# Kernel tuning notes

Measured on AMD Instinct MI355X. Metric: run time of the kernel, lower is better.

The kernel has to match this reference:

```python
import jax, jax.numpy as jnp
import numpy as np

IN_CH, OUT_CH, KS = 64, 128, 3
GRID, DEG = 8, 3
STRIDE, PAD = 1, 1
SIZE = IN_CH * KS * KS            # 576
NCOEF = GRID + DEG                # 11
GRID_RANGE = (-1.0, 1.0)


def _xavier_uniform(key, shape):
    fan_out, fan_in = shape
    a = float(np.sqrt(6.0 / (fan_in + fan_out)))
    return jax.random.uniform(key, shape, minval=-a, maxval=a, dtype=jnp.float32)


def setup_inputs() -> dict:
    key = jax.random.key(0)
    k1, k2, k3 = jax.random.split(key, 3)
    x = jax.random.normal(k1, (8, IN_CH, 32, 32), dtype=jnp.float32)
    # non-trainable knot grid, one row per unfolded feature
    knots = jnp.tile(jnp.linspace(GRID_RANGE[0], GRID_RANGE[1], GRID + 1, dtype=jnp.float32)[None, :], (SIZE, 1))
    coeff = 0.1 * jax.random.normal(k2, (OUT_CH, SIZE, NCOEF), dtype=jnp.float32)
    base_weights = _xavier_uniform(k3, (OUT_CH, SIZE))
    spline_weights = jnp.ones((OUT_CH, SIZE), dtype=jnp.float32)
    return {"x": x, "knots": knots, "coeff": coeff,
            "base_weights": base_weights, "spline_weights": spline_weights}


def bspline_basis(x, grid, k):
    # x: (S, P) evaluation points; grid: (S, G+1) knots. Returns (S, G+k, P).
    h = (grid[:, -1:] - grid[:, :1]) / (grid.shape[1] - 1)
    left = grid[:, :1] - h * jnp.arange(k, 0, -1, dtype=x.dtype)
    right = grid[:, -1:] + h * jnp.arange(1, k + 1, dtype=x.dtype)
    g = jnp.concatenate([left, grid, right], axis=1)  # (S, G+1+2k)
    xe = x[:, None, :]
    B = ((xe >= g[:, :-1, None]) & (xe < g[:, 1:, None])).astype(x.dtype)
    for d in range(1, k + 1):  # de Boor recursion over fixed degree
        B = ((xe - g[:, :-(d + 1), None]) / (g[:, d:-1, None] - g[:, :-(d + 1), None]) * B[:, :-1]
             + (g[:, d + 1:, None] - xe) / (g[:, d + 1:, None] - g[:, 1:-d, None]) * B[:, 1:])
    return B


def _unfold(x):
    # torch F.unfold with channel-major (c, kh, kw) feature ordering
    N, C, H, W = x.shape
    xp = jnp.pad(x, ((0, 0), (0, 0), (PAD, PAD), (PAD, PAD)))
    Hp = (H + 2 * PAD - KS) // STRIDE + 1
    Wp = (W + 2 * PAD - KS) // STRIDE + 1
    patches = jnp.stack([xp[:, :, i:i + STRIDE * Hp:STRIDE, j:j + STRIDE * Wp:STRIDE]
                         for i in range(KS) for j in range(KS)], axis=2)  # (N, C, KS*KS, Hp, Wp)
    L = Hp * Wp
    u = patches.reshape(N, SIZE, L)              # (N, size, L)
    u = jnp.transpose(u, (1, 0, 2)).reshape(SIZE, N * L)  # (size, N*L), col = n*L + l
    return u, Hp, Wp


def reference(x, knots, coeff, base_weights, spline_weights):
    N = x.shape[0]
    u, Hp, Wp = _unfold(x)                                   # (size, P)
    base = base_weights @ jax.nn.silu(u)                     # (Cout, P)
    B = bspline_basis(u, knots, DEG)                         # (size, ncoef, P)
    eff = spline_weights[:, :, None] * coeff                 # (Cout, size, ncoef)
    spl = jnp.einsum('csj,sjp->cp', eff, B)                  # (Cout, P)
    out = (base + spl).reshape(OUT_CH, N, Hp, Wp)
    return jnp.transpose(out, (1, 0, 2, 3))                  # (N, Cout, Hp, Wp)
```

## Files before the change

kernel.cpp:

```cpp
#include <hip/hip_runtime.h>


typedef __attribute__((ext_vector_type(8))) short bf16x8;
typedef __attribute__((ext_vector_type(4))) float f32x4;
typedef __attribute__((ext_vector_type(16))) float f32x16;
typedef __attribute__((ext_vector_type(4))) unsigned short u16x4;

#define WSWZ_BYTES 1769472
#define PHI_OFF    WSWZ_BYTES
#define PHI_BYTES  14205696

__device__ __forceinline__ short f2bf(float f) {
    union { float f; unsigned u; } c; c.f = f;
    unsigned r = c.u + 0x7fffu + ((c.u >> 16) & 1u);
    return (short)(r >> 16);
}
__device__ __forceinline__ float bf2f(unsigned short u) {
    union { unsigned u; float f; } c; c.u = ((unsigned)u) << 16;
    return c.f;
}

__global__ void kan_prep(const float* __restrict__ coeff,
                         const float* __restrict__ basew,
                         const float* __restrict__ splw,
                         const float* __restrict__ x,
                         short* __restrict__ Wswz,
                         short* __restrict__ Phi) {
    __shared__ float coeffL[6336];
    __shared__ float basewL[576];
    __shared__ float splwL[576];
    __shared__ unsigned short xs[64 * 32];
    const int t = threadIdx.x;

    if (blockIdx.x < 272) {
        const int rowid = blockIdx.x;
        const int n     = rowid / 34;
        const int ypad  = rowid - n * 34;
        const int y     = ypad - 1;
        const bool yvalid = (y >= 0 && y < 32);

        if (yvalid) {
#pragma unroll
            for (int it = 0; it < 2; ++it) {
                int cg = t + it * 256;
                int ci = cg >> 3, q = cg & 7;
                f32x4 v = *(const f32x4*)(x + (((n * 64 + ci) * 32 + y) * 32 + q * 4));
                u16x4 p;
                p.x = (unsigned short)f2bf(v.x); p.y = (unsigned short)f2bf(v.y);
                p.z = (unsigned short)f2bf(v.z); p.w = (unsigned short)f2bf(v.w);
                *(u16x4*)&xs[ci * 32 + q * 4] = p;
            }
        }
        __syncthreads();

        const size_t rowbase = (size_t)rowid * 12 * 2176;
        for (int it = t; it < 272; it += 256) {
            int xp = it >> 3, cch = it & 7, c0 = cch << 3;
            bool interior = yvalid && (xp >= 1 && xp <= 32);
            int px = xp - 1;
            int pxc = px < 0 ? 0 : (px > 31 ? 31 : px);
            bf16x8 packs[12];
#pragma unroll
            for (int j = 0; j < 8; ++j) {
                float v = interior ? bf2f(xs[(c0 + j) * 32 + pxc]) : 0.f;
                float tt = 4.f * v + 7.f;
                int   i0 = -100;
                float b0 = 0.f, b1 = 0.f, b2 = 0.f, b3 = 0.f;
                if (tt >= 0.f && tt < 14.f) {
                    i0 = (int)tt;
                    float fr  = tt - (float)i0;
                    float omf = 1.f - fr;
                    float fr2 = fr * fr, fr3 = fr2 * fr;
                    b0 = omf * omf * omf * (1.f / 6.f);
                    b1 = (3.f * fr3 - 6.f * fr2 + 4.f) * (1.f / 6.f);
                    b2 = (-3.f * fr3 + 3.f * fr2 + 3.f * fr + 1.f) * (1.f / 6.f);
                    b3 = fr3 * (1.f / 6.f);
                }
                float silu = v * __builtin_amdgcn_rcpf(1.f + __expf(-v));
                packs[0][j] = f2bf(silu);
#pragma unroll
                for (int f = 1; f < 12; ++f) {
                    int jj = f - 1;
                    float val = 0.f;
                    val = (jj == i0 - 3) ? b0 : val;
                    val = (jj == i0 - 2) ? b1 : val;
                    val = (jj == i0 - 1) ? b2 : val;
                    val = (jj == i0    ) ? b3 : val;
                    packs[f][j] = f2bf(val);
                }
            }
            int swz = (cch ^ (xp & 7)) << 3;
#pragma unroll
            for (int f = 0; f < 12; ++f)
                *(bf16x8*)&Phi[rowbase + (size_t)f * 2176 + xp * 64 + swz] = packs[f];
        }
    } else {
        const int co = blockIdx.x - 272;
        const float* crow = coeff + co * 6336;
        for (int i = t; i < 6336; i += 256) coeffL[i] = crow[i];
        for (int i = t; i < 576; i += 256) {
            basewL[i] = basew[co * 576 + i];
            splwL[i]  = splw[co * 576 + i];
        }
        __syncthreads();
        const int cb = co >> 5, lm = co & 31;
        for (int c = t; c < 864; c += 256) {
            int kk16 = c >> 1, kh = c & 1;
            int f  = kk16 / 36;
            int rm = kk16 - f * 36;
            int tap = rm >> 2, q = rm & 3;
            bf16x8 pack;
#pragma unroll
            for (int j = 0; j < 8; ++j) {
                int ci = q * 16 + kh * 8 + j;
                int s  = ci * 9 + tap;
                float v = (f == 0) ? basewL[s] : splwL[s] * coeffL[s * 11 + (f - 1)];
                pack[j] = f2bf(v);
            }
            *(bf16x8*)(Wswz + (size_t)((kk16 * 4 + cb) * 64 + kh * 32 + lm) * 8) = pack;
        }
    }
}

__global__ __launch_bounds__(512, 1)
void kan_gemm2(const short* __restrict__ Phi,
               const short* __restrict__ Wswz,
               float* __restrict__ out) {
    __shared__ __align__(16) char Bbuf[2 * 69632];

    const int t  = threadIdx.x;
    const int w8 = t >> 6;
    const int cb = w8 & 1;
    const int fq = w8 >> 1;
    const int l  = t & 63;
    const int ln = l & 31;
    const int kh = l >> 5;

    const int ch    = blockIdx.x >> 7;
    const int ptile = blockIdx.x & 127;
    const int n     = ptile >> 4;
    const int y0    = (ptile & 15) << 1;
    const int cbg   = ch * 2 + cb;

    const char* phiB = (const char*)Phi;
    const int rowPlane = (n * 34 + y0) * 12;
    auto stage = [&](int r, int buf) {
#pragma unroll
        for (int k = 0; k < 9; ++k) {
            int i = t + k * 512;
            if (i < 4352) {
                int sfq = i / 1088;
                int rem = i - sfq * 1088;
                int row = rem / 272;
                int m   = rem - row * 272;
                const char* s = phiB + (size_t)(rowPlane + row * 12 + sfq * 3 + r) * 4352 + m * 16;
                __builtin_amdgcn_global_load_lds(
                    (const __attribute__((address_space(1))) unsigned int*)s,
                    (__attribute__((address_space(3))) unsigned int*)(Bbuf + buf * 69632 + i * 16),
                    16, 0, 0);
            }
        }
    };

    stage(0, 0);
    __syncthreads();

    f32x16 acc[2];
#pragma unroll
    for (int pb = 0; pb < 2; ++pb)
#pragma unroll
        for (int r = 0; r < 16; ++r)
            acc[pb][r] = 0.f;

    const short* Abase = Wswz + (size_t)cbg * 512 + (size_t)l * 8;

#pragma unroll 1
    for (int r = 0; r < 3; ++r) {
        const int buf = r & 1;
        if (r < 2) stage(r + 1, buf ^ 1);

        const short* B0 = (const short*)(Bbuf + buf * 69632 + fq * 17408);
        const int kbase = (fq * 3 + r) * 36;
#pragma unroll
        for (int q = 0; q < 4; ++q) {
#pragma unroll
            for (int dx = 0; dx < 3; ++dx) {
                bf16x8 a0 = *(const bf16x8*)(Abase + (size_t)(kbase + (0 * 3 + dx) * 4 + q) * 2048);
                bf16x8 a1 = *(const bf16x8*)(Abase + (size_t)(kbase + (1 * 3 + dx) * 4 + q) * 2048);
                bf16x8 a2 = *(const bf16x8*)(Abase + (size_t)(kbase + (2 * 3 + dx) * 4 + q) * 2048);
                const int c   = q * 2 + kh;
                const int key = (ln + dx) & 7;
                const int colb = (ln + dx) * 64 + ((c ^ key) << 3);
                bf16x8 b0 = *(const bf16x8*)&B0[0 * 2176 + colb];
                bf16x8 b1 = *(const bf16x8*)&B0[1 * 2176 + colb];
                bf16x8 b2 = *(const bf16x8*)&B0[2 * 2176 + colb];
                bf16x8 b3 = *(const bf16x8*)&B0[3 * 2176 + colb];
                acc[0] = __builtin_amdgcn_mfma_f32_32x32x16_bf16(a0, b0, acc[0], 0, 0, 0);
                acc[1] = __builtin_amdgcn_mfma_f32_32x32x16_bf16(a0, b1, acc[1], 0, 0, 0);
                acc[0] = __builtin_amdgcn_mfma_f32_32x32x16_bf16(a1, b1, acc[0], 0, 0, 0);
                acc[1] = __builtin_amdgcn_mfma_f32_32x32x16_bf16(a1, b2, acc[1], 0, 0, 0);
                acc[0] = __builtin_amdgcn_mfma_f32_32x32x16_bf16(a2, b2, acc[0], 0, 0, 0);
                acc[1] = __builtin_amdgcn_mfma_f32_32x32x16_bf16(a2, b3, acc[1], 0, 0, 0);
            }
        }
        __syncthreads();
    }

    float* ex = (float*)Bbuf;
    if (fq != 0) {
        const int slot = (fq - 1) * 2 + cb;
#pragma unroll
        for (int pb = 0; pb < 2; ++pb)
#pragma unroll
            for (int r = 0; r < 16; ++r) {
                int v = pb * 16 + r;
                ex[slot * 2048 + l * 32 + ((v + l) & 31)] = acc[pb][r];
            }
    }
    __syncthreads();
    if (fq == 0) {
#pragma unroll
        for (int s = 0; s < 3; ++s)
#pragma unroll
            for (int pb = 0; pb < 2; ++pb)
#pragma unroll
                for (int r = 0; r < 16; ++r) {
                    int v = pb * 16 + r;
                    acc[pb][r] += ex[(s * 2 + cb) * 2048 + l * 32 + ((v + l) & 31)];
                }

#pragma unroll
        for (int pb = 0; pb < 2; ++pb) {
            int y = y0 + pb;
#pragma unroll
            for (int r = 0; r < 16; ++r) {
                int row = (r & 3) + 8 * (r >> 2) + 4 * kh;
                int co  = cbg * 32 + row;
                out[((size_t)(n * 128 + co) * 32 + y) * 32 + ln] = acc[pb][r];
            }
        }
    }
}

extern "C" void kernel_launch(void* const* d_in, const int* in_sizes, int n_in,
                              void* d_out, int out_size, void* d_ws, size_t ws_size,
                              hipStream_t stream) {
    const float* x     = (const float*)d_in[0];
    const float* coeff = (const float*)d_in[2];
    const float* basew = (const float*)d_in[3];
    const float* splw  = (const float*)d_in[4];
    float* out = (float*)d_out;

    short* Wswz = (short*)d_ws;
    short* Phi  = (short*)((char*)d_ws + PHI_OFF);

    kan_prep<<<400, 256, 0, stream>>>(coeff, basew, splw, x, Wswz, Phi);
    kan_gemm2<<<256, 512, 0, stream>>>(Phi, Wswz, out);
}
```

Before: 102.7 us.

## Fuse basis expansion into GEMM kernel, dropping the materialized Phi buffer

Each GEMM block now loads its four padded input rows, converts them to bf16 in shared memory, and computes the SiLU and B-spline basis values on the fly into LDS for each of the three feature rounds. The prep kernel that wrote a ~14 MB Phi tensor to global memory and the async global-to-LDS staging are removed, leaving a weights-only prep kernel. This cuts global memory traffic but moves basis computation into the GEMM blocks and serializes it with the MFMA loop, since there is no double buffering, and each block recomputes halo rows.

```diff
diff --git a/kernel.cpp b/kernel.cpp
--- a/kernel.cpp
+++ b/kernel.cpp
@@ -6,10 +6,6 @@
 typedef __attribute__((ext_vector_type(16))) float f32x16;
 typedef __attribute__((ext_vector_type(4))) unsigned short u16x4;
 
-#define WSWZ_BYTES 1769472
-#define PHI_OFF    WSWZ_BYTES
-#define PHI_BYTES  14205696
-
 __device__ __forceinline__ short f2bf(float f) {
     union { float f; unsigned u; } c; c.f = f;
     unsigned r = c.u + 0x7fffu + ((c.u >> 16) & 1u);
@@ -20,49 +16,96 @@
     return c.f;
 }
 
-__global__ void kan_prep(const float* __restrict__ coeff,
-                         const float* __restrict__ basew,
-                         const float* __restrict__ splw,
-                         const float* __restrict__ x,
-                         short* __restrict__ Wswz,
-                         short* __restrict__ Phi) {
+__global__ void kan_weights(const float* __restrict__ coeff,
+                            const float* __restrict__ basew,
+                            const float* __restrict__ splw,
+                            short* __restrict__ Wswz) {
     __shared__ float coeffL[6336];
     __shared__ float basewL[576];
     __shared__ float splwL[576];
-    __shared__ unsigned short xs[64 * 32];
-    const int t = threadIdx.x;
-
-    if (blockIdx.x < 272) {
-        const int rowid = blockIdx.x;
-        const int n     = rowid / 34;
-        const int ypad  = rowid - n * 34;
-        const int y     = ypad - 1;
-        const bool yvalid = (y >= 0 && y < 32);
-
-        if (yvalid) {
-#pragma unroll
-            for (int it = 0; it < 2; ++it) {
-                int cg = t + it * 256;
-                int ci = cg >> 3, q = cg & 7;
-                f32x4 v = *(const f32x4*)(x + (((n * 64 + ci) * 32 + y) * 32 + q * 4));
-                u16x4 p;
-                p.x = (unsigned short)f2bf(v.x); p.y = (unsigned short)f2bf(v.y);
-                p.z = (unsigned short)f2bf(v.z); p.w = (unsigned short)f2bf(v.w);
-                *(u16x4*)&xs[ci * 32 + q * 4] = p;
-            }
-        }
-        __syncthreads();
-
-        const size_t rowbase = (size_t)rowid * 12 * 2176;
-        for (int it = t; it < 272; it += 256) {
-            int xp = it >> 3, cch = it & 7, c0 = cch << 3;
-            bool interior = yvalid && (xp >= 1 && xp <= 32);
-            int px = xp - 1;
-            int pxc = px < 0 ? 0 : (px > 31 ? 31 : px);
-            bf16x8 packs[12];
+    const int co = blockIdx.x;
+    const int t  = threadIdx.x;
+    const float* crow = coeff + co * 6336;
+    for (int i = t; i < 6336; i += 256) coeffL[i] = crow[i];
+    for (int i = t; i < 576; i += 256) {
+        basewL[i] = basew[co * 576 + i];
+        splwL[i]  = splw[co * 576 + i];
+    }
+    __syncthreads();
+    const int cb = co >> 5, lm = co & 31;
+    for (int c = t; c < 864; c += 256) {
+        int kk16 = c >> 1, kh = c & 1;
+        int f  = kk16 / 36;
+        int rm = kk16 - f * 36;
+        int tap = rm >> 2, q = rm & 3;
+        bf16x8 pack;
+#pragma unroll
+        for (int j = 0; j < 8; ++j) {
+            int ci = q * 16 + kh * 8 + j;
+            int s  = ci * 9 + tap;
+            float v = (f == 0) ? basewL[s] : splwL[s] * coeffL[s * 11 + (f - 1)];
+            pack[j] = f2bf(v);
+        }
+        *(bf16x8*)(Wswz + (size_t)((kk16 * 4 + cb) * 64 + kh * 32 + lm) * 8) = pack;
+    }
+}
+
+__global__ __launch_bounds__(512, 1)
+void kan_gemm3(const float* __restrict__ x,
+               const short* __restrict__ Wswz,
+               float* __restrict__ out) {
+    __shared__ unsigned short xs[4 * 64 * 36];
+    __shared__ __align__(16) short Bs[4 * 8704];
+
+    const int t  = threadIdx.x;
+    const int w8 = t >> 6;
+    const int cb = w8 & 1;
+    const int fq = w8 >> 1;
+    const int l  = t & 63;
+    const int ln = l & 31;
+    const int kh = l >> 5;
+
+    const int ch    = blockIdx.x >> 7;
+    const int ptile = blockIdx.x & 127;
+    const int n     = ptile >> 4;
+    const int y0    = (ptile & 15) << 1;
+    const int cbg   = ch * 2 + cb;
+
+#pragma unroll
+    for (int it = 0; it < 4; ++it) {
+        int cg = t + it * 512;
+        int rr = cg >> 9, ci = (cg >> 3) & 63, q = cg & 7;
+        int y  = y0 - 1 + rr;
+        f32x4 v = {0.f, 0.f, 0.f, 0.f};
+        if (y >= 0 && y < 32)
+            v = *(const f32x4*)(x + (((n * 64 + ci) * 32 + y) * 32 + q * 4));
+        u16x4 p;
+        p.x = (unsigned short)f2bf(v.x); p.y = (unsigned short)f2bf(v.y);
+        p.z = (unsigned short)f2bf(v.z); p.w = (unsigned short)f2bf(v.w);
+        *(u16x4*)&xs[(rr * 64 + ci) * 36 + q * 4] = p;
+    }
+    __syncthreads();
+
+    f32x16 acc[2];
+#pragma unroll
+    for (int pb = 0; pb < 2; ++pb)
+#pragma unroll
+        for (int r = 0; r < 16; ++r)
+            acc[pb][r] = 0.f;
+
+    const short* Abase = Wswz + (size_t)cbg * 512 + (size_t)l * 8;
+
+#pragma unroll 1
+    for (int r = 0; r < 3; ++r) {
+        for (int it = t; it < 1088; it += 512) {
+            int rr  = it / 272;
+            int rem = it - rr * 272;
+            int xp = rem >> 3, cch = rem & 7, c0 = cch << 3;
+            bool interior = (xp >= 1 && xp <= 32);
+            bf16x8 packs[4];
 #pragma unroll
             for (int j = 0; j < 8; ++j) {
-                float v = interior ? bf2f(xs[(c0 + j) * 32 + pxc]) : 0.f;
+                float v = interior ? bf2f(xs[(rr * 64 + c0 + j) * 36 + (xp - 1)]) : 0.f;
                 float tt = 4.f * v + 7.f;
                 int   i0 = -100;
                 float b0 = 0.f, b1 = 0.f, b2 = 0.f, b3 = 0.f;
@@ -76,110 +119,31 @@
                     b2 = (-3.f * fr3 + 3.f * fr2 + 3.f * fr + 1.f) * (1.f / 6.f);
                     b3 = fr3 * (1.f / 6.f);
                 }
-                float silu = v * __builtin_amdgcn_rcpf(1.f + __expf(-v));
-                packs[0][j] = f2bf(silu);
-#pragma unroll
-                for (int f = 1; f < 12; ++f) {
-                    int jj = f - 1;
-                    float val = 0.f;
-                    val = (jj == i0 - 3) ? b0 : val;
-                    val = (jj == i0 - 2) ? b1 : val;
-                    val = (jj == i0 - 1) ? b2 : val;
-                    val = (jj == i0    ) ? b3 : val;
-                    packs[f][j] = f2bf(val);
+#pragma unroll
+                for (int sfq = 0; sfq < 4; ++sfq) {
+                    int f = sfq * 3 + r;
+                    float val;
+                    if (f == 0) {
+                        val = v * __builtin_amdgcn_rcpf(1.f + __expf(-v));
+                    } else {
+                        int jj = f - 1;
+                        val = 0.f;
+                        val = (jj == i0 - 3) ? b0 : val;
+                        val = (jj == i0 - 2) ? b1 : val;
+                        val = (jj == i0 - 1) ? b2 : val;
+                        val = (jj == i0    ) ? b3 : val;
+                    }
+                    packs[sfq][j] = f2bf(val);
                 }
             }
-            int swz = (cch ^ (xp & 7)) << 3;
-#pragma unroll
-            for (int f = 0; f < 12; ++f)
-                *(bf16x8*)&Phi[rowbase + (size_t)f * 2176 + xp * 64 + swz] = packs[f];
-        }
-    } else {
-        const int co = blockIdx.x - 272;
-        const float* crow = coeff + co * 6336;
-        for (int i = t; i < 6336; i += 256) coeffL[i] = crow[i];
-        for (int i = t; i < 576; i += 256) {
-            basewL[i] = basew[co * 576 + i];
-            splwL[i]  = splw[co * 576 + i];
+            int base = rr * 2176 + xp * 64 + ((cch ^ (xp & 7)) << 3);
+#pragma unroll
+            for (int sfq = 0; sfq < 4; ++sfq)
+                *(bf16x8*)&Bs[sfq * 8704 + base] = packs[sfq];
         }
         __syncthreads();
-        const int cb = co >> 5, lm = co & 31;
-        for (int c = t; c < 864; c += 256) {
-            int kk16 = c >> 1, kh = c & 1;
-            int f  = kk16 / 36;
-            int rm = kk16 - f * 36;
-            int tap = rm >> 2, q = rm & 3;
-            bf16x8 pack;
-#pragma unroll
-            for (int j = 0; j < 8; ++j) {
-                int ci = q * 16 + kh * 8 + j;
-                int s  = ci * 9 + tap;
-                float v = (f == 0) ? basewL[s] : splwL[s] * coeffL[s * 11 + (f - 1)];
-                pack[j] = f2bf(v);
-            }
-            *(bf16x8*)(Wswz + (size_t)((kk16 * 4 + cb) * 64 + kh * 32 + lm) * 8) = pack;
-        }
-    }
-}
-
-__global__ __launch_bounds__(512, 1)
-void kan_gemm2(const short* __restrict__ Phi,
-               const short* __restrict__ Wswz,
-               float* __restrict__ out) {
-    __shared__ __align__(16) char Bbuf[2 * 69632];
-
-    const int t  = threadIdx.x;
-    const int w8 = t >> 6;
-    const int cb = w8 & 1;
-    const int fq = w8 >> 1;
-    const int l  = t & 63;
-    const int ln = l & 31;
-    const int kh = l >> 5;
-
-    const int ch    = blockIdx.x >> 7;
-    const int ptile = blockIdx.x & 127;
-    const int n     = ptile >> 4;
-    const int y0    = (ptile & 15) << 1;
-    const int cbg   = ch * 2 + cb;
-
-    const char* phiB = (const char*)Phi;
-    const int rowPlane = (n * 34 + y0) * 12;
-    auto stage = [&](int r, int buf) {
-#pragma unroll
-        for (int k = 0; k < 9; ++k) {
-            int i = t + k * 512;
-            if (i < 4352) {
-                int sfq = i / 1088;
-                int rem = i - sfq * 1088;
-                int row = rem / 272;
-                int m   = rem - row * 272;
-                const char* s = phiB + (size_t)(rowPlane + row * 12 + sfq * 3 + r) * 4352 + m * 16;
-                __builtin_amdgcn_global_load_lds(
-                    (const __attribute__((address_space(1))) unsigned int*)s,
-                    (__attribute__((address_space(3))) unsigned int*)(Bbuf + buf * 69632 + i * 16),
-                    16, 0, 0);
-            }
-        }
-    };
-
-    stage(0, 0);
-    __syncthreads();
-
-    f32x16 acc[2];
-#pragma unroll
-    for (int pb = 0; pb < 2; ++pb)
-#pragma unroll
-        for (int r = 0; r < 16; ++r)
-            acc[pb][r] = 0.f;
-
-    const short* Abase = Wswz + (size_t)cbg * 512 + (size_t)l * 8;
-
-#pragma unroll 1
-    for (int r = 0; r < 3; ++r) {
-        const int buf = r & 1;
-        if (r < 2) stage(r + 1, buf ^ 1);
-
-        const short* B0 = (const short*)(Bbuf + buf * 69632 + fq * 17408);
+
+        const short* B0 = Bs + fq * 8704;
         const int kbase = (fq * 3 + r) * 36;
 #pragma unroll
         for (int q = 0; q < 4; ++q) {
@@ -206,7 +170,7 @@
         __syncthreads();
     }
 
-    float* ex = (float*)Bbuf;
+    float* ex = (float*)Bs;
     if (fq != 0) {
         const int slot = (fq - 1) * 2 + cb;
 #pragma unroll
@@ -252,8 +216,7 @@
     float* out = (float*)d_out;
 
     short* Wswz = (short*)d_ws;
-    short* Phi  = (short*)((char*)d_ws + PHI_OFF);
-
-    kan_prep<<<400, 256, 0, stream>>>(coeff, basew, splw, x, Wswz, Phi);
-    kan_gemm2<<<256, 512, 0, stream>>>(Phi, Wswz, out);
-}
+
+    kan_weights<<<128, 256, 0, stream>>>(coeff, basew, splw, Wswz);
+    kan_gemm3<<<256, 512, 0, stream>>>(x, Wswz, out);
+}
```

Result: slower. 111.9 us (+9.0%).

## Split GEMM into smaller single-buffered blocks with two blocks per CU

Applied to the files above, without the earlier changes.

The GEMM kernel changes from 512-thread blocks covering two 32-channel groups to 256-thread blocks covering one, launched as 512 blocks with launch bounds allowing two blocks per CU. LDS staging drops from double-buffered to single-buffered, with a sync after each load, so per-block shared memory halves and two blocks can co-reside. The aim is to hide load latency through inter-block occupancy instead of intra-block prefetch. In exchange, each Phi tile is now loaded twice (once per channel block), and loads no longer overlap compute within a block.

```diff
diff --git a/kernel.cpp b/kernel.cpp
--- a/kernel.cpp
+++ b/kernel.cpp
@@ -122,32 +122,40 @@
     }
 }
 
-__global__ __launch_bounds__(512, 1)
-void kan_gemm2(const short* __restrict__ Phi,
-               const short* __restrict__ Wswz,
-               float* __restrict__ out) {
-    __shared__ __align__(16) char Bbuf[2 * 69632];
+__global__ __launch_bounds__(256, 2)
+void kan_gemm2b(const short* __restrict__ Phi,
+                const short* __restrict__ Wswz,
+                float* __restrict__ out) {
+    __shared__ __align__(16) short Bs[4 * 8704];
 
     const int t  = threadIdx.x;
-    const int w8 = t >> 6;
-    const int cb = w8 & 1;
-    const int fq = w8 >> 1;
+    const int fq = t >> 6;
     const int l  = t & 63;
     const int ln = l & 31;
     const int kh = l >> 5;
 
-    const int ch    = blockIdx.x >> 7;
+    const int cq    = blockIdx.x >> 7;
     const int ptile = blockIdx.x & 127;
     const int n     = ptile >> 4;
     const int y0    = (ptile & 15) << 1;
-    const int cbg   = ch * 2 + cb;
 
     const char* phiB = (const char*)Phi;
     const int rowPlane = (n * 34 + y0) * 12;
-    auto stage = [&](int r, int buf) {
-#pragma unroll
-        for (int k = 0; k < 9; ++k) {
-            int i = t + k * 512;
+
+    f32x16 acc[2];
+#pragma unroll
+    for (int pb = 0; pb < 2; ++pb)
+#pragma unroll
+        for (int r = 0; r < 16; ++r)
+            acc[pb][r] = 0.f;
+
+    const short* Abase = Wswz + (size_t)cq * 512 + (size_t)l * 8;
+
+#pragma unroll 1
+    for (int r = 0; r < 3; ++r) {
+#pragma unroll
+        for (int k = 0; k < 17; ++k) {
+            int i = t + k * 256;
             if (i < 4352) {
                 int sfq = i / 1088;
                 int rem = i - sfq * 1088;
@@ -156,30 +164,13 @@
                 const char* s = phiB + (size_t)(rowPlane + row * 12 + sfq * 3 + r) * 4352 + m * 16;
                 __builtin_amdgcn_global_load_lds(
                     (const __attribute__((address_space(1))) unsigned int*)s,
-                    (__attribute__((address_space(3))) unsigned int*)(Bbuf + buf * 69632 + i * 16),
+                    (__attribute__((address_space(3))) unsigned int*)((char*)Bs + i * 16),
                     16, 0, 0);
             }
         }
-    };
-
-    stage(0, 0);
-    __syncthreads();
-
-    f32x16 acc[2];
-#pragma unroll
-    for (int pb = 0; pb < 2; ++pb)
-#pragma unroll
-        for (int r = 0; r < 16; ++r)
-            acc[pb][r] = 0.f;
-
-    const short* Abase = Wswz + (size_t)cbg * 512 + (size_t)l * 8;
-
-#pragma unroll 1
-    for (int r = 0; r < 3; ++r) {
-        const int buf = r & 1;
-        if (r < 2) stage(r + 1, buf ^ 1);
-
-        const short* B0 = (const short*)(Bbuf + buf * 69632 + fq * 17408);
+        __syncthreads();
+
+        const short* B0 = Bs + fq * 8704;
         const int kbase = (fq * 3 + r) * 36;
 #pragma unroll
         for (int q = 0; q < 4; ++q) {
@@ -206,9 +197,9 @@
         __syncthreads();
     }
 
-    float* ex = (float*)Bbuf;
+    float* ex = (float*)Bs;
     if (fq != 0) {
-        const int slot = (fq - 1) * 2 + cb;
+        const int slot = fq - 1;
 #pragma unroll
         for (int pb = 0; pb < 2; ++pb)
 #pragma unroll
@@ -226,7 +217,7 @@
 #pragma unroll
                 for (int r = 0; r < 16; ++r) {
                     int v = pb * 16 + r;
-                    acc[pb][r] += ex[(s * 2 + cb) * 2048 + l * 32 + ((v + l) & 31)];
+                    acc[pb][r] += ex[s * 2048 + l * 32 + ((v + l) & 31)];
                 }
 
 #pragma unroll
@@ -235,7 +226,7 @@
 #pragma unroll
             for (int r = 0; r < 16; ++r) {
                 int row = (r & 3) + 8 * (r >> 2) + 4 * kh;
-                int co  = cbg * 32 + row;
+                int co  = cq * 32 + row;
                 out[((size_t)(n * 128 + co) * 32 + y) * 32 + ln] = acc[pb][r];
             }
         }
@@ -255,5 +246,5 @@
     short* Phi  = (short*)((char*)d_ws + PHI_OFF);
 
     kan_prep<<<400, 256, 0, stream>>>(coeff, basew, splw, x, Wswz, Phi);
-    kan_gemm2<<<256, 512, 0, stream>>>(Phi, Wswz, out);
-}
+    kan_gemm2b<<<512, 256, 0, stream>>>(Phi, Wswz, out);
+}
```

Result: slower. 105.4 us (+2.6%).

## Preload weight fragments into registers and unroll the staged GEMM pipeline

Applied to the files above, without the earlier changes.

The GEMM kernel now loads all 36 weight (A) fragments for the next stage into registers ahead of each compute phase, instead of issuing global loads inside the MFMA loop. The three-stage loop is unrolled by hand so these loads overlap with MFMA work and the LDS staging of Phi. Launch bounds are raised to allow two blocks per CU. Holding 36 bf16x8 fragments (about 144 VGPRs) under the tighter register limit risks spills, and with 256 blocks the extra occupancy may not be used.

```diff
diff --git a/kernel.cpp b/kernel.cpp
--- a/kernel.cpp
+++ b/kernel.cpp
@@ -122,11 +122,11 @@
     }
 }
 
-__global__ __launch_bounds__(512, 1)
-void kan_gemm2(const short* __restrict__ Phi,
-               const short* __restrict__ Wswz,
-               float* __restrict__ out) {
-    __shared__ __align__(16) char Bbuf[2 * 69632];
+__global__ __launch_bounds__(512, 2)
+void kan_gemm2p(const short* __restrict__ Phi,
+                const short* __restrict__ Wswz,
+                float* __restrict__ out) {
+    __shared__ __align__(16) short Bs[2][4 * 8704];
 
     const int t  = threadIdx.x;
     const int w8 = t >> 6;
@@ -144,6 +144,8 @@
 
     const char* phiB = (const char*)Phi;
     const int rowPlane = (n * 34 + y0) * 12;
+    const short* Abase = Wswz + (size_t)cbg * 512 + (size_t)l * 8;
+
     auto stage = [&](int r, int buf) {
 #pragma unroll
         for (int k = 0; k < 9; ++k) {
@@ -156,14 +158,24 @@
                 const char* s = phiB + (size_t)(rowPlane + row * 12 + sfq * 3 + r) * 4352 + m * 16;
                 __builtin_amdgcn_global_load_lds(
                     (const __attribute__((address_space(1))) unsigned int*)s,
-                    (__attribute__((address_space(3))) unsigned int*)(Bbuf + buf * 69632 + i * 16),
+                    (__attribute__((address_space(3))) unsigned int*)((char*)&Bs[buf][0] + i * 16),
                     16, 0, 0);
             }
         }
     };
 
-    stage(0, 0);
-    __syncthreads();
+    bf16x8 ag[36];
+    auto preloadA = [&](int r) {
+        const int kbase = (fq * 3 + r) * 36;
+#pragma unroll
+        for (int g = 0; g < 36; ++g) {
+            int q  = g / 9;
+            int rm = g - q * 9;
+            int dx = rm / 3;
+            int dy = rm - dx * 3;
+            ag[g] = *(const bf16x8*)(Abase + (size_t)(kbase + (dy * 3 + dx) * 4 + q) * 2048);
+        }
+    };
 
     f32x16 acc[2];
 #pragma unroll
@@ -172,22 +184,12 @@
         for (int r = 0; r < 16; ++r)
             acc[pb][r] = 0.f;
 
-    const short* Abase = Wswz + (size_t)cbg * 512 + (size_t)l * 8;
-
-#pragma unroll 1
-    for (int r = 0; r < 3; ++r) {
-        const int buf = r & 1;
-        if (r < 2) stage(r + 1, buf ^ 1);
-
-        const short* B0 = (const short*)(Bbuf + buf * 69632 + fq * 17408);
-        const int kbase = (fq * 3 + r) * 36;
+    auto compute = [&](const short* B0) {
 #pragma unroll
         for (int q = 0; q < 4; ++q) {
 #pragma unroll
             for (int dx = 0; dx < 3; ++dx) {
-                bf16x8 a0 = *(const bf16x8*)(Abase + (size_t)(kbase + (0 * 3 + dx) * 4 + q) * 2048);
-                bf16x8 a1 = *(const bf16x8*)(Abase + (size_t)(kbase + (1 * 3 + dx) * 4 + q) * 2048);
-                bf16x8 a2 = *(const bf16x8*)(Abase + (size_t)(kbase + (2 * 3 + dx) * 4 + q) * 2048);
+                const int g0 = q * 9 + dx * 3;
                 const int c   = q * 2 + kh;
                 const int key = (ln + dx) & 7;
                 const int colb = (ln + dx) * 64 + ((c ^ key) << 3);
@@ -195,18 +197,34 @@
                 bf16x8 b1 = *(const bf16x8*)&B0[1 * 2176 + colb];
                 bf16x8 b2 = *(const bf16x8*)&B0[2 * 2176 + colb];
                 bf16x8 b3 = *(const bf16x8*)&B0[3 * 2176 + colb];
-                acc[0] = __builtin_amdgcn_mfma_f32_32x32x16_bf16(a0, b0, acc[0], 0, 0, 0);
-                acc[1] = __builtin_amdgcn_mfma_f32_32x32x16_bf16(a0, b1, acc[1], 0, 0, 0);
-                acc[0] = __builtin_amdgcn_mfma_f32_32x32x16_bf16(a1, b1, acc[0], 0, 0, 0);
-                acc[1] = __builtin_amdgcn_mfma_f32_32x32x16_bf16(a1, b2, acc[1], 0, 0, 0);
-                acc[0] = __builtin_amdgcn_mfma_f32_32x32x16_bf16(a2, b2, acc[0], 0, 0, 0);
-                acc[1] = __builtin_amdgcn_mfma_f32_32x32x16_bf16(a2, b3, acc[1], 0, 0, 0);
-            }
-        }
-        __syncthreads();
-    }
-
-    float* ex = (float*)Bbuf;
+                acc[0] = __builtin_amdgcn_mfma_f32_32x32x16_bf16(ag[g0 + 0], b0, acc[0], 0, 0, 0);
+                acc[1] = __builtin_amdgcn_mfma_f32_32x32x16_bf16(ag[g0 + 0], b1, acc[1], 0, 0, 0);
+                acc[0] = __builtin_amdgcn_mfma_f32_32x32x16_bf16(ag[g0 + 1], b1, acc[0], 0, 0, 0);
+                acc[1] = __builtin_amdgcn_mfma_f32_32x32x16_bf16(ag[g0 + 1], b2, acc[1], 0, 0, 0);
+                acc[0] = __builtin_amdgcn_mfma_f32_32x32x16_bf16(ag[g0 + 2], b2, acc[0], 0, 0, 0);
+                acc[1] = __builtin_amdgcn_mfma_f32_32x32x16_bf16(ag[g0 + 2], b3, acc[1], 0, 0, 0);
+            }
+        }
+    };
+
+    preloadA(0);
+    stage(0, 0);
+    __syncthreads();
+
+    stage(1, 1);
+    compute(&Bs[0][fq * 8704]);
+    preloadA(1);
+    __syncthreads();
+
+    stage(2, 0);
+    compute(&Bs[1][fq * 8704]);
+    preloadA(2);
+    __syncthreads();
+
+    compute(&Bs[0][fq * 8704]);
+
+    __syncthreads();
+    float* ex = (float*)&Bs[1][0];
     if (fq != 0) {
         const int slot = (fq - 1) * 2 + cb;
 #pragma unroll
@@ -255,5 +273,5 @@
     short* Phi  = (short*)((char*)d_ws + PHI_OFF);
 
     kan_prep<<<400, 256, 0, stream>>>(coeff, basew, splw, x, Wswz, Phi);
-    kan_gemm2<<<256, 512, 0, stream>>>(Phi, Wswz, out);
-}
+    kan_gemm2p<<<256, 512, 0, stream>>>(Phi, Wswz, out);
+}
```

Result: faster. 96.74 us (-5.9%).
